# Optimization experiments

Measured on AMD Instinct MI355X. Metric: run time of the kernel, lower is better.

Reference implementation:

```python
import jax, jax.numpy as jnp
import numpy as np

HEADS = 16
D_MODEL = 1024
GROUP = 4
SEQ = 2048
HEAD_DIM = D_MODEL // HEADS          # 64
KV_HEADS = HEADS // GROUP            # 4


def rope_tables(head_dim, seq_len, base=10000.0):
    # NOTE: faithful to source: exp = -2*arange(0,d,2)/d  (steps of 2 -> base^{-4j/d})
    exp = -2.0 * jnp.arange(0, head_dim, 2, dtype=jnp.float32) / head_dim
    thetas = jnp.power(base, exp)                       # [d/2]
    m = jnp.arange(seq_len, dtype=jnp.float32)          # [S]
    freq = jnp.outer(m, thetas)                         # [S, d/2]
    return jnp.cos(freq), jnp.sin(freq)


def apply_rope(x, cos, sin):
    # x: [B,S,H,D]; complex rotation on consecutive pairs
    B, S, H, D = x.shape
    xr = x.reshape(B, S, H, D // 2, 2)
    x0, x1 = xr[..., 0], xr[..., 1]
    c = cos[None, :S, None, :]
    s = sin[None, :S, None, :]
    out = jnp.stack([x0 * c - x1 * s, x0 * s + x1 * c], axis=-1)
    return out.reshape(B, S, H, D)


def setup_inputs() -> dict:
    key = jax.random.key(0)
    ks = jax.random.split(key, 8)
    B = 1
    q = jax.random.normal(ks[0], (B, SEQ, D_MODEL), dtype=jnp.float32)
    k = jax.random.normal(ks[1], (B, SEQ, D_MODEL), dtype=jnp.float32)
    v = jax.random.normal(ks[2], (B, SEQ, D_MODEL), dtype=jnp.float32)
    mask = jnp.tril(jnp.ones((SEQ, SEQ), dtype=jnp.int32))[None]  # causal [B,S,S]
    sc = 0.02
    Wq = jax.random.normal(ks[3], (D_MODEL, D_MODEL), dtype=jnp.float32) * sc
    Wk = jax.random.normal(ks[4], (D_MODEL, D_MODEL // GROUP), dtype=jnp.float32) * sc
    Wv = jax.random.normal(ks[5], (D_MODEL, D_MODEL // GROUP), dtype=jnp.float32) * sc
    Wo = jax.random.normal(ks[6], (D_MODEL, D_MODEL), dtype=jnp.float32) * sc
    bq = jnp.zeros((D_MODEL,), jnp.float32)
    bk = jnp.zeros((D_MODEL // GROUP,), jnp.float32)
    bv = jnp.zeros((D_MODEL // GROUP,), jnp.float32)
    bo = jnp.zeros((D_MODEL,), jnp.float32)
    return {"q": q, "k": k, "v": v, "mask": mask, "Wq": Wq, "bq": bq,
            "Wk": Wk, "bk": bk, "Wv": Wv, "bv": bv, "Wo": Wo, "bo": bo}


def reference(q, k, v, mask, Wq, bq, Wk, bk, Wv, bv, Wo, bo):
    B, S, _ = q.shape
    cos, sin = rope_tables(HEAD_DIM, S)
    qh = (q @ Wq + bq).reshape(B, S, HEADS, HEAD_DIM)
    kh = (k @ Wk + bk).reshape(B, S, KV_HEADS, HEAD_DIM)
    vh = (v @ Wv + bv).reshape(B, S, KV_HEADS, HEAD_DIM)
    qh = apply_rope(qh, cos, sin)
    kh = apply_rope(kh, cos, sin)
    qh = qh.transpose(0, 2, 1, 3)                       # [B,H,S,D]
    kh = kh.transpose(0, 2, 1, 3)                       # [B,Hkv,S,D]
    vh = vh.transpose(0, 2, 1, 3)
    # torch .repeat tiles: query head j attends kv head j % KV_HEADS
    kh = jnp.tile(kh, (1, GROUP, 1, 1))                 # [B,H,S,D]
    vh = jnp.tile(vh, (1, GROUP, 1, 1))
    scores = jnp.einsum('bhqd,bhkd->bhqk', qh, kh) / jnp.sqrt(
        jnp.asarray(HEAD_DIM, dtype=qh.dtype))
    scores = jnp.where(mask[:, None, :, :] == 0, -jnp.inf, scores)
    attn = jax.nn.softmax(scores, axis=-1)
    out = jnp.einsum('bhqk,bhkd->bhqd', attn, vh)
    out = out.transpose(0, 2, 1, 3).reshape(B, S, D_MODEL)
    return out @ Wo + bo
```

## Files before the change

### kernel.cpp

```cpp
#include <hip/hip_runtime.h>
#include <hip/hip_bf16.h>
#include <math.h>


#define SEQ 2048
#define DM 1024
#define HD 64

using u16 = unsigned short;
typedef __attribute__((ext_vector_type(8))) short bf16x8;
typedef __attribute__((ext_vector_type(4))) float f32x4;

#define QSCALE 0.18033688011112042f

__device__ __forceinline__ u16 f2b(float f) {
    union { float f; unsigned int i; } v; v.f = f;
    unsigned int u = v.i;
    return (u16)((u + 0x7fffu + ((u >> 16) & 1u)) >> 16);
}
__device__ __forceinline__ u16 f2b_fast(float f) {
    union { float f; unsigned int i; } v; v.f = f;
    return (u16)((v.i + 0x8000u) >> 16);
}

__global__ __launch_bounds__(256) void prep_kernel(
    const float* __restrict__ qin, const float* __restrict__ kin, const float* __restrict__ vin,
    const float* __restrict__ Wq, const float* __restrict__ Wk,
    const float* __restrict__ Wv, const float* __restrict__ Wo,
    u16* __restrict__ Xq, u16* __restrict__ Xk, u16* __restrict__ Xv,
    u16* __restrict__ Wt, u16* __restrict__ wot)
{
    const int b = blockIdx.x;
    const int t = threadIdx.x;

    if (b < 640) {
        __shared__ short T[64][72];
        const float* W; u16* dst; int N, t0, rowoff;
        if (b < 256)      { W = Wq; dst = Wt;  N = 1024; t0 = b;       rowoff = 0; }
        else if (b < 320) { W = Wk; dst = Wt;  N = 256;  t0 = b - 256; rowoff = 1024; }
        else if (b < 384) { W = Wv; dst = Wt;  N = 256;  t0 = b - 320; rowoff = 1280; }
        else              { W = Wo; dst = wot; N = 1024; t0 = b - 384; rowoff = 0; }
        const int ntn = N >> 6;
        const int k0 = (t0 / ntn) * 64, n0 = (t0 % ntn) * 64;
        const int r = t >> 4, c4 = (t & 15) * 4;
        #pragma unroll
        for (int rr = 0; rr < 4; ++rr) {
            const int k = r + rr * 16;
            float4 w4 = *reinterpret_cast<const float4*>(W + (size_t)(k0 + k) * N + n0 + c4);
            T[c4 + 0][k] = (short)f2b(w4.x);
            T[c4 + 1][k] = (short)f2b(w4.y);
            T[c4 + 2][k] = (short)f2b(w4.z);
            T[c4 + 3][k] = (short)f2b(w4.w);
        }
        __syncthreads();
        const int n = t >> 2, ck = (t & 3) * 16;
        u16* dp = dst + (size_t)(rowoff + n0 + n) * DM + k0 + ck;
        *reinterpret_cast<bf16x8*>(dp)     = *reinterpret_cast<const bf16x8*>(&T[n][ck]);
        *reinterpret_cast<bf16x8*>(dp + 8) = *reinterpret_cast<const bf16x8*>(&T[n][ck + 8]);
    } else {
        const int idx = b - 640;
        const int which = idx >> 8;
        const int ib = idx & 255;
        const float* src = (which == 0) ? qin : (which == 1) ? kin : vin;
        u16* dst = (which == 0) ? Xq : (which == 1) ? Xk : Xv;
        const size_t base = (size_t)ib * 8192 + (size_t)t * 32;
        #pragma unroll
        for (int c = 0; c < 4; ++c) {
            float4 x0 = *reinterpret_cast<const float4*>(src + base + c * 8);
            float4 x1 = *reinterpret_cast<const float4*>(src + base + c * 8 + 4);
            bf16x8 o;
            o[0] = (short)f2b(x0.x); o[1] = (short)f2b(x0.y);
            o[2] = (short)f2b(x0.z); o[3] = (short)f2b(x0.w);
            o[4] = (short)f2b(x1.x); o[5] = (short)f2b(x1.y);
            o[6] = (short)f2b(x1.z); o[7] = (short)f2b(x1.w);
            *reinterpret_cast<bf16x8*>(dst + base + c * 8) = o;
        }
    }
}

__global__ __launch_bounds__(256) void proj_mfma(
    const u16* __restrict__ Xq, const u16* __restrict__ Xk, const u16* __restrict__ Xv,
    const u16* __restrict__ Wt,
    const float* __restrict__ bq, const float* __restrict__ bk, const float* __restrict__ bv,
    u16* __restrict__ Qr, u16* __restrict__ Kr, u16* __restrict__ Vrt)
{
    const int n0 = blockIdx.x * 64, m0 = blockIdx.y * 64;
    const int zone = (n0 < 1024) ? 0 : (n0 < 1280) ? 1 : 2;
    const u16* __restrict__ Az = (zone == 0) ? Xq : (zone == 1) ? Xk : Xv;

    __shared__ short As[64][72];
    __shared__ short Bs[64][72];

    const int t = threadIdx.x;
    const int w = t >> 6, lane = t & 63, lm = lane & 15, quad = lane >> 4;
    const int sr = t >> 2, sc = (t & 3) * 16;

    f32x4 acc[4] = { {0,0,0,0}, {0,0,0,0}, {0,0,0,0}, {0,0,0,0} };

    for (int k0 = 0; k0 < DM; k0 += 64) {
        const u16* ap = Az + (size_t)(m0 + sr) * DM + k0 + sc;
        *reinterpret_cast<bf16x8*>(&As[sr][sc])     = *reinterpret_cast<const bf16x8*>(ap);
        *reinterpret_cast<bf16x8*>(&As[sr][sc + 8]) = *reinterpret_cast<const bf16x8*>(ap + 8);
        const u16* bp = Wt + (size_t)(n0 + sr) * DM + k0 + sc;
        *reinterpret_cast<bf16x8*>(&Bs[sr][sc])     = *reinterpret_cast<const bf16x8*>(bp);
        *reinterpret_cast<bf16x8*>(&Bs[sr][sc + 8]) = *reinterpret_cast<const bf16x8*>(bp + 8);
        __syncthreads();
        bf16x8 af0 = *reinterpret_cast<const bf16x8*>(&As[16 * w + lm][quad * 8]);
        bf16x8 af1 = *reinterpret_cast<const bf16x8*>(&As[16 * w + lm][32 + quad * 8]);
        #pragma unroll
        for (int nb = 0; nb < 4; ++nb) {
            bf16x8 b0 = *reinterpret_cast<const bf16x8*>(&Bs[16 * nb + lm][quad * 8]);
            bf16x8 b1 = *reinterpret_cast<const bf16x8*>(&Bs[16 * nb + lm][32 + quad * 8]);
            acc[nb] = __builtin_amdgcn_mfma_f32_16x16x32_bf16(af0, b0, acc[nb], 0, 0, 0);
            acc[nb] = __builtin_amdgcn_mfma_f32_16x16x32_bf16(af1, b1, acc[nb], 0, 0, 0);
        }
        __syncthreads();
    }

    const float* __restrict__ bias = (zone == 0) ? bq : (zone == 1) ? bk : bv;
    const int nbase = (zone == 0) ? n0 : (zone == 1) ? (n0 - 1024) : (n0 - 1280);
    const int head = nbase >> 6;
    #pragma unroll
    for (int nb = 0; nb < 4; ++nb) {
        const int d = 16 * nb + lm;
        const float bvv = bias[nbase + d];
        float vals[4];
        #pragma unroll
        for (int r = 0; r < 4; ++r) vals[r] = acc[nb][r] + bvv;
        if (zone != 2) {
            const int pi = d >> 1;
            const float theta = exp2f(-0.8304820237f * (float)pi);
            const bool odd = (lm & 1);
            const float sca = (zone == 0) ? QSCALE : 1.0f;
            #pragma unroll
            for (int r = 0; r < 4; ++r) {
                const int m = m0 + 16 * w + quad * 4 + r;
                float sn, cs;
                sincosf((float)m * theta, &sn, &cs);
                float x  = vals[r];
                float xp = __shfl_xor(x, 1);
                vals[r] = (odd ? (xp * sn + x * cs) : (x * cs - xp * sn)) * sca;
            }
            u16* op = (zone == 0 ? Qr : Kr) + (size_t)head * SEQ * HD;
            #pragma unroll
            for (int r = 0; r < 4; ++r) {
                const int m = m0 + 16 * w + quad * 4 + r;
                op[(size_t)m * HD + d] = f2b(vals[r]);
            }
        } else {
            u16 pk[4];
            #pragma unroll
            for (int r = 0; r < 4; ++r) pk[r] = f2b(vals[r]);
            u16* vp = Vrt + ((size_t)head * HD + d) * SEQ + m0 + 16 * w + quad * 4;
            *reinterpret_cast<uint2*>(vp) = *reinterpret_cast<uint2*>(pk);
        }
    }
}

__global__ __launch_bounds__(256) void attn_mfma(
    const u16* __restrict__ Qr, const u16* __restrict__ Kr, const u16* __restrict__ Vrt,
    u16* __restrict__ AO)
{
    const int h  = blockIdx.x;
    const int qy = blockIdx.y;
    const int qt = (qy < 16) ? (2 * qy) : (63 - 2 * qy);
    const int kvh = h & 3;

    __shared__ short Qs[64][72];
    __shared__ short Ks[2][64][72];
    __shared__ short Vt[64][136];
    __shared__ short Ps[64][136];
    __shared__ float Lred[4][64];

    const int t = threadIdx.x;
    const int w = t >> 6, lane = t & 63, lm = lane & 15, quad = lane >> 4;
    const int sr = t >> 2, sc = (t & 3) * 16;
    const int colb = (sc >> 4) * 32;

    {
        const u16* qp = Qr + ((size_t)h * SEQ + qt * 64 + sr) * HD + sc;
        *reinterpret_cast<bf16x8*>(&Qs[sr][sc])     = *reinterpret_cast<const bf16x8*>(qp);
        *reinterpret_cast<bf16x8*>(&Qs[sr][sc + 8]) = *reinterpret_cast<const bf16x8*>(qp + 8);
    }
    __syncthreads();
    bf16x8 bq[4][2];
    #pragma unroll
    for (int nb = 0; nb < 4; ++nb) {
        bq[nb][0] = *reinterpret_cast<const bf16x8*>(&Qs[16 * nb + lm][quad * 8]);
        bq[nb][1] = *reinterpret_cast<const bf16x8*>(&Qs[16 * nb + lm][32 + quad * 8]);
    }

    f32x4 O[4][4];
    #pragma unroll
    for (int i = 0; i < 4; ++i)
        #pragma unroll
        for (int j = 0; j < 4; ++j) O[i][j] = (f32x4){0.f, 0.f, 0.f, 0.f};
    float lp[4] = { 0.f, 0.f, 0.f, 0.f };

    const int ntile = qt + 1;
    const u16* kbase = Kr  + ((size_t)kvh * SEQ + sr) * HD + sc;
    const u16* vbase = Vrt + ((size_t)kvh * HD  + sr) * SEQ + sc;

    for (int u = 0; u < ntile; u += 2) {
        const bool has1 = (u + 1 < ntile);
        {
            const u16* kp0 = kbase + (size_t)u * 64 * HD;
            *reinterpret_cast<bf16x8*>(&Ks[0][sr][sc])     = *reinterpret_cast<const bf16x8*>(kp0);
            *reinterpret_cast<bf16x8*>(&Ks[0][sr][sc + 8]) = *reinterpret_cast<const bf16x8*>(kp0 + 8);
            const u16* vp0 = vbase + (size_t)u * 64;
            *reinterpret_cast<bf16x8*>(&Vt[sr][colb])      = *reinterpret_cast<const bf16x8*>(vp0);
            *reinterpret_cast<bf16x8*>(&Vt[sr][colb + 8])  = *reinterpret_cast<const bf16x8*>(vp0 + 8);
            if (has1) {
                const u16* kp1 = kbase + (size_t)(u + 1) * 64 * HD;
                *reinterpret_cast<bf16x8*>(&Ks[1][sr][sc])     = *reinterpret_cast<const bf16x8*>(kp1);
                *reinterpret_cast<bf16x8*>(&Ks[1][sr][sc + 8]) = *reinterpret_cast<const bf16x8*>(kp1 + 8);
                const u16* vp1 = vbase + (size_t)(u + 1) * 64;
                *reinterpret_cast<bf16x8*>(&Vt[sr][colb + 16]) = *reinterpret_cast<const bf16x8*>(vp1);
                *reinterpret_cast<bf16x8*>(&Vt[sr][colb + 24]) = *reinterpret_cast<const bf16x8*>(vp1 + 8);
            } else {
                bf16x8 z = {0,0,0,0,0,0,0,0};
                *reinterpret_cast<bf16x8*>(&Vt[sr][colb + 16]) = z;
                *reinterpret_cast<bf16x8*>(&Vt[sr][colb + 24]) = z;
            }
        }
        __syncthreads();

        #pragma unroll
        for (int tp = 0; tp < 2; ++tp) {
            const int kt = u + tp;
            if (tp == 1 && !has1) {
                const uint2 z2 = make_uint2(0u, 0u);
                #pragma unroll
                for (int nb = 0; nb < 4; ++nb)
                    *reinterpret_cast<uint2*>(&Ps[16 * nb + lm][w * 32 + 16 + quad * 4]) = z2;
                continue;
            }
            const bf16x8 ak0 = *reinterpret_cast<const bf16x8*>(&Ks[tp][16 * w + lm][quad * 8]);
            const bf16x8 ak1 = *reinterpret_cast<const bf16x8*>(&Ks[tp][16 * w + lm][32 + quad * 8]);
            const bool diag = (kt == qt);
            #pragma unroll
            for (int nb = 0; nb < 4; ++nb) {
                f32x4 ss = { 0.f, 0.f, 0.f, 0.f };
                ss = __builtin_amdgcn_mfma_f32_16x16x32_bf16(ak0, bq[nb][0], ss, 0, 0, 0);
                ss = __builtin_amdgcn_mfma_f32_16x16x32_bf16(ak1, bq[nb][1], ss, 0, 0, 0);
                u16 pk[4];
                #pragma unroll
                for (int r = 0; r < 4; ++r) {
                    float sv = ss[r];
                    if (diag && (16 * w + quad * 4 + r > 16 * nb + lm)) sv = -INFINITY;
                    float e = __builtin_amdgcn_exp2f(fminf(sv, 126.f));
                    lp[nb] += e;
                    pk[r] = f2b_fast(e);
                }
                *reinterpret_cast<uint2*>(&Ps[16 * nb + lm][w * 32 + tp * 16 + quad * 4]) =
                    *reinterpret_cast<uint2*>(pk);
            }
        }

        #pragma unroll
        for (int db = 0; db < 4; ++db) {
            const bf16x8 av = *reinterpret_cast<const bf16x8*>(&Vt[16 * db + lm][w * 32 + quad * 8]);
            #pragma unroll
            for (int nb = 0; nb < 4; ++nb) {
                const bf16x8 bp = *reinterpret_cast<const bf16x8*>(&Ps[16 * nb + lm][w * 32 + quad * 8]);
                O[db][nb] = __builtin_amdgcn_mfma_f32_16x16x32_bf16(av, bp, O[db][nb], 0, 0, 0);
            }
        }
        __syncthreads();
    }

    #pragma unroll
    for (int nb = 0; nb < 4; ++nb) {
        lp[nb] += __shfl_xor(lp[nb], 16);
        lp[nb] += __shfl_xor(lp[nb], 32);
    }
    if (quad == 0) {
        #pragma unroll
        for (int nb = 0; nb < 4; ++nb) Lred[w][16 * nb + lm] = lp[nb];
    }

    float* Sf = reinterpret_cast<float*>(&Ps[0][0]);
    #pragma unroll
    for (int ph = 0; ph < 4; ++ph) {
        __syncthreads();
        if (w == ph) {
            #pragma unroll
            for (int db = 0; db < 4; ++db)
                #pragma unroll
                for (int nb = 0; nb < 4; ++nb)
                    #pragma unroll
                    for (int r = 0; r < 4; ++r) {
                        const int d = 16 * db + quad * 4 + r, q = 16 * nb + lm;
                        const float v = O[db][nb][r];
                        Sf[q * 68 + d] = (ph == 0) ? v : (Sf[q * 68 + d] + v);
                    }
        }
    }
    __syncthreads();

    {
        const int q = t >> 2, dc = (t & 3) * 16;
        const float linv = 1.0f / (Lred[0][q] + Lred[1][q] + Lred[2][q] + Lred[3][q]);
        u16 pk[16];
        #pragma unroll
        for (int j = 0; j < 16; ++j)
            pk[j] = f2b(Sf[q * 68 + dc + j] * linv);
        u16* op = AO + (size_t)(qt * 64 + q) * DM + h * HD + dc;
        *reinterpret_cast<bf16x8*>(op)     = *reinterpret_cast<const bf16x8*>(pk);
        *reinterpret_cast<bf16x8*>(op + 8) = *reinterpret_cast<const bf16x8*>(pk + 8);
    }
}

__global__ __launch_bounds__(256) void oproj_mfma(
    const u16* __restrict__ AO, const u16* __restrict__ wot,
    const float* __restrict__ bo, float* __restrict__ out)
{
    __shared__ short As[64][72];
    __shared__ short Bs[64][72];
    const int t = threadIdx.x;
    const int w = t >> 6, lane = t & 63, lm = lane & 15, quad = lane >> 4;
    const int m0 = blockIdx.y * 64, n0 = blockIdx.x * 64;
    const int sr = t >> 2, sc = (t & 3) * 16;

    f32x4 acc[4] = { {0,0,0,0}, {0,0,0,0}, {0,0,0,0}, {0,0,0,0} };

    for (int k0 = 0; k0 < DM; k0 += 64) {
        const u16* ap = AO + (size_t)(m0 + sr) * DM + k0 + sc;
        *reinterpret_cast<bf16x8*>(&As[sr][sc])     = *reinterpret_cast<const bf16x8*>(ap);
        *reinterpret_cast<bf16x8*>(&As[sr][sc + 8]) = *reinterpret_cast<const bf16x8*>(ap + 8);
        const u16* bp = wot + (size_t)(n0 + sr) * DM + k0 + sc;
        *reinterpret_cast<bf16x8*>(&Bs[sr][sc])     = *reinterpret_cast<const bf16x8*>(bp);
        *reinterpret_cast<bf16x8*>(&Bs[sr][sc + 8]) = *reinterpret_cast<const bf16x8*>(bp + 8);
        __syncthreads();
        bf16x8 af0 = *reinterpret_cast<const bf16x8*>(&As[16 * w + lm][quad * 8]);
        bf16x8 af1 = *reinterpret_cast<const bf16x8*>(&As[16 * w + lm][32 + quad * 8]);
        #pragma unroll
        for (int nb = 0; nb < 4; ++nb) {
            bf16x8 b0 = *reinterpret_cast<const bf16x8*>(&Bs[16 * nb + lm][quad * 8]);
            bf16x8 b1 = *reinterpret_cast<const bf16x8*>(&Bs[16 * nb + lm][32 + quad * 8]);
            acc[nb] = __builtin_amdgcn_mfma_f32_16x16x32_bf16(af0, b0, acc[nb], 0, 0, 0);
            acc[nb] = __builtin_amdgcn_mfma_f32_16x16x32_bf16(af1, b1, acc[nb], 0, 0, 0);
        }
        __syncthreads();
    }

    #pragma unroll
    for (int nb = 0; nb < 4; ++nb) {
        const int dl = 16 * nb + lm;
        const float bv = bo[n0 + dl];
        #pragma unroll
        for (int r = 0; r < 4; ++r) {
            const int m = m0 + 16 * w + quad * 4 + r;
            out[(size_t)m * DM + n0 + dl] = acc[nb][r] + bv;
        }
    }
}

extern "C" void kernel_launch(void* const* d_in, const int* in_sizes, int n_in,
                              void* d_out, int out_size, void* d_ws, size_t ws_size,
                              hipStream_t stream)
{
    const float* q  = (const float*)d_in[0];
    const float* k  = (const float*)d_in[1];
    const float* v  = (const float*)d_in[2];
    const float* Wq = (const float*)d_in[4];
    const float* bq = (const float*)d_in[5];
    const float* Wk = (const float*)d_in[6];
    const float* bk = (const float*)d_in[7];
    const float* Wv = (const float*)d_in[8];
    const float* bv = (const float*)d_in[9];
    const float* Wo = (const float*)d_in[10];
    const float* bo = (const float*)d_in[11];
    float* out = (float*)d_out;

    u16* Xq  = (u16*)d_ws;
    u16* Xk  = Xq  + (size_t)SEQ * DM;
    u16* Xv  = Xk  + (size_t)SEQ * DM;
    u16* Wt  = Xv  + (size_t)SEQ * DM;
    u16* wot = Wt  + (size_t)1536 * 1024;
    u16* Qr  = wot + (size_t)1024 * 1024;
    u16* Kr  = Qr  + (size_t)16 * SEQ * HD;
    u16* Vrt = Kr  + (size_t)4 * SEQ * HD;
    u16* AO  = Vrt + (size_t)4 * SEQ * HD;

    hipLaunchKernelGGL(prep_kernel, dim3(1408), dim3(256), 0, stream,
                       q, k, v, Wq, Wk, Wv, Wo, Xq, Xk, Xv, Wt, wot);
    hipLaunchKernelGGL(proj_mfma, dim3(24, 32), dim3(256), 0, stream,
                       Xq, Xk, Xv, Wt, bq, bk, bv, Qr, Kr, Vrt);
    hipLaunchKernelGGL(attn_mfma, dim3(16, 32), dim3(256), 0, stream,
                       Qr, Kr, Vrt, AO);
    hipLaunchKernelGGL(oproj_mfma, dim3(16, 32), dim3(256), 0, stream,
                       AO, wot, bo, out);
}
```

Before: 184.0 us.

## Restructure attention into paired-tile 512-thread blocks and prefetch GEMM tiles

Both GEMM kernels now prefetch the next K tile into registers while computing from a double-buffered LDS tile, which hides global load latency. The attention kernel is rewritten so each 512-thread block processes two complementary query tiles (qy and 31-qy) with one team of four waves each, for balanced causal work. Each wave owns 16 query rows and keeps its own P buffer, so the cross-wave O reduction through shared memory goes away. V is now stored in an interleaved permuted order to match the new PV MFMA operand layout. The risks are higher register and LDS pressure and correctness depending on that permuted V layout.

```diff
diff --git a/kernel.cpp b/kernel.cpp
--- a/kernel.cpp
+++ b/kernel.cpp
@@ -88,8 +88,8 @@
     const int zone = (n0 < 1024) ? 0 : (n0 < 1280) ? 1 : 2;
     const u16* __restrict__ Az = (zone == 0) ? Xq : (zone == 1) ? Xk : Xv;
 
-    __shared__ short As[64][72];
-    __shared__ short Bs[64][72];
+    __shared__ short As[2][64][72];
+    __shared__ short Bs[2][64][72];
 
     const int t = threadIdx.x;
     const int w = t >> 6, lane = t & 63, lm = lane & 15, quad = lane >> 4;
@@ -97,20 +97,32 @@
 
     f32x4 acc[4] = { {0,0,0,0}, {0,0,0,0}, {0,0,0,0}, {0,0,0,0} };
 
+    const u16* ap_ = Az + (size_t)(m0 + sr) * DM + sc;
+    const u16* bp_ = Wt + (size_t)(n0 + sr) * DM + sc;
+    bf16x8 aR0 = *reinterpret_cast<const bf16x8*>(ap_);
+    bf16x8 aR1 = *reinterpret_cast<const bf16x8*>(ap_ + 8);
+    bf16x8 bR0 = *reinterpret_cast<const bf16x8*>(bp_);
+    bf16x8 bR1 = *reinterpret_cast<const bf16x8*>(bp_ + 8);
+
     for (int k0 = 0; k0 < DM; k0 += 64) {
-        const u16* ap = Az + (size_t)(m0 + sr) * DM + k0 + sc;
-        *reinterpret_cast<bf16x8*>(&As[sr][sc])     = *reinterpret_cast<const bf16x8*>(ap);
-        *reinterpret_cast<bf16x8*>(&As[sr][sc + 8]) = *reinterpret_cast<const bf16x8*>(ap + 8);
-        const u16* bp = Wt + (size_t)(n0 + sr) * DM + k0 + sc;
-        *reinterpret_cast<bf16x8*>(&Bs[sr][sc])     = *reinterpret_cast<const bf16x8*>(bp);
-        *reinterpret_cast<bf16x8*>(&Bs[sr][sc + 8]) = *reinterpret_cast<const bf16x8*>(bp + 8);
-        __syncthreads();
-        bf16x8 af0 = *reinterpret_cast<const bf16x8*>(&As[16 * w + lm][quad * 8]);
-        bf16x8 af1 = *reinterpret_cast<const bf16x8*>(&As[16 * w + lm][32 + quad * 8]);
+        const int buf = (k0 >> 6) & 1;
+        *reinterpret_cast<bf16x8*>(&As[buf][sr][sc])     = aR0;
+        *reinterpret_cast<bf16x8*>(&As[buf][sr][sc + 8]) = aR1;
+        *reinterpret_cast<bf16x8*>(&Bs[buf][sr][sc])     = bR0;
+        *reinterpret_cast<bf16x8*>(&Bs[buf][sr][sc + 8]) = bR1;
+        if (k0 + 64 < DM) {
+            aR0 = *reinterpret_cast<const bf16x8*>(ap_ + k0 + 64);
+            aR1 = *reinterpret_cast<const bf16x8*>(ap_ + k0 + 72);
+            bR0 = *reinterpret_cast<const bf16x8*>(bp_ + k0 + 64);
+            bR1 = *reinterpret_cast<const bf16x8*>(bp_ + k0 + 72);
+        }
+        __syncthreads();
+        bf16x8 af0 = *reinterpret_cast<const bf16x8*>(&As[buf][16 * w + lm][quad * 8]);
+        bf16x8 af1 = *reinterpret_cast<const bf16x8*>(&As[buf][16 * w + lm][32 + quad * 8]);
         #pragma unroll
         for (int nb = 0; nb < 4; ++nb) {
-            bf16x8 b0 = *reinterpret_cast<const bf16x8*>(&Bs[16 * nb + lm][quad * 8]);
-            bf16x8 b1 = *reinterpret_cast<const bf16x8*>(&Bs[16 * nb + lm][32 + quad * 8]);
+            bf16x8 b0 = *reinterpret_cast<const bf16x8*>(&Bs[buf][16 * nb + lm][quad * 8]);
+            bf16x8 b1 = *reinterpret_cast<const bf16x8*>(&Bs[buf][16 * nb + lm][32 + quad * 8]);
             acc[nb] = __builtin_amdgcn_mfma_f32_16x16x32_bf16(af0, b0, acc[nb], 0, 0, 0);
             acc[nb] = __builtin_amdgcn_mfma_f32_16x16x32_bf16(af1, b1, acc[nb], 0, 0, 0);
         }
@@ -132,6 +144,7 @@
             const float theta = exp2f(-0.8304820237f * (float)pi);
             const bool odd = (lm & 1);
             const float sca = (zone == 0) ? QSCALE : 1.0f;
+            u16* op = (zone == 0 ? Qr : Kr) + (size_t)head * SEQ * HD;
             #pragma unroll
             for (int r = 0; r < 4; ++r) {
                 const int m = m0 + 16 * w + quad * 4 + r;
@@ -139,175 +152,122 @@
                 sincosf((float)m * theta, &sn, &cs);
                 float x  = vals[r];
                 float xp = __shfl_xor(x, 1);
-                vals[r] = (odd ? (xp * sn + x * cs) : (x * cs - xp * sn)) * sca;
-            }
-            u16* op = (zone == 0 ? Qr : Kr) + (size_t)head * SEQ * HD;
+                float o  = (odd ? (xp * sn + x * cs) : (x * cs - xp * sn)) * sca;
+                op[(size_t)m * HD + d] = f2b(o);
+            }
+        } else {
+            u16* vp = Vrt + ((size_t)head * HD + d) * SEQ;
             #pragma unroll
             for (int r = 0; r < 4; ++r) {
                 const int m = m0 + 16 * w + quad * 4 + r;
-                op[(size_t)m * HD + d] = f2b(vals[r]);
-            }
-        } else {
-            u16 pk[4];
-            #pragma unroll
-            for (int r = 0; r < 4; ++r) pk[r] = f2b(vals[r]);
-            u16* vp = Vrt + ((size_t)head * HD + d) * SEQ + m0 + 16 * w + quad * 4;
-            *reinterpret_cast<uint2*>(vp) = *reinterpret_cast<uint2*>(pk);
-        }
-    }
-}
-
-__global__ __launch_bounds__(256) void attn_mfma(
+                const int within = m & 63;
+                const int pos = (m & ~63) + 4 * (within & 15) + (within >> 4);
+                vp[pos] = f2b(vals[r]);
+            }
+        }
+    }
+}
+
+__global__ __launch_bounds__(512) void attn_mfma(
     const u16* __restrict__ Qr, const u16* __restrict__ Kr, const u16* __restrict__ Vrt,
     u16* __restrict__ AO)
 {
     const int h  = blockIdx.x;
     const int qy = blockIdx.y;
-    const int qt = (qy < 16) ? (2 * qy) : (63 - 2 * qy);
     const int kvh = h & 3;
 
-    __shared__ short Qs[64][72];
-    __shared__ short Ks[2][64][72];
-    __shared__ short Vt[64][136];
-    __shared__ short Ps[64][136];
-    __shared__ float Lred[4][64];
+    __shared__ u16 Ks[2][64][72];
+    __shared__ u16 Vt[2][64][72];
+    __shared__ u16 Ps[8][16][76];
 
     const int t = threadIdx.x;
     const int w = t >> 6, lane = t & 63, lm = lane & 15, quad = lane >> 4;
-    const int sr = t >> 2, sc = (t & 3) * 16;
-    const int colb = (sc >> 4) * 32;
+    const int team = w >> 2, wt = w & 3;
+    const int qt  = team ? (31 - qy) : qy;
+    const int qtb = 31 - qy;
 
     {
-        const u16* qp = Qr + ((size_t)h * SEQ + qt * 64 + sr) * HD + sc;
-        *reinterpret_cast<bf16x8*>(&Qs[sr][sc])     = *reinterpret_cast<const bf16x8*>(qp);
-        *reinterpret_cast<bf16x8*>(&Qs[sr][sc + 8]) = *reinterpret_cast<const bf16x8*>(qp + 8);
-    }
-    __syncthreads();
-    bf16x8 bq[4][2];
-    #pragma unroll
-    for (int nb = 0; nb < 4; ++nb) {
-        bq[nb][0] = *reinterpret_cast<const bf16x8*>(&Qs[16 * nb + lm][quad * 8]);
-        bq[nb][1] = *reinterpret_cast<const bf16x8*>(&Qs[16 * nb + lm][32 + quad * 8]);
-    }
-
-    f32x4 O[4][4];
-    #pragma unroll
-    for (int i = 0; i < 4; ++i)
-        #pragma unroll
-        for (int j = 0; j < 4; ++j) O[i][j] = (f32x4){0.f, 0.f, 0.f, 0.f};
+        const int row = lane >> 2, c = (lane & 3) * 16;
+        const u16* qp = Qr + ((size_t)h * SEQ + qt * 64 + wt * 16 + row) * HD + c;
+        *reinterpret_cast<bf16x8*>(&Ps[w][row][c])     = *reinterpret_cast<const bf16x8*>(qp);
+        *reinterpret_cast<bf16x8*>(&Ps[w][row][c + 8]) = *reinterpret_cast<const bf16x8*>(qp + 8);
+    }
+    const bf16x8 aq0 = *reinterpret_cast<const bf16x8*>(&Ps[w][lm][quad * 8]);
+    const bf16x8 aq1 = *reinterpret_cast<const bf16x8*>(&Ps[w][lm][32 + quad * 8]);
+
+    f32x4 O[4] = { {0,0,0,0}, {0,0,0,0}, {0,0,0,0}, {0,0,0,0} };
     float lp[4] = { 0.f, 0.f, 0.f, 0.f };
 
-    const int ntile = qt + 1;
-    const u16* kbase = Kr  + ((size_t)kvh * SEQ + sr) * HD + sc;
-    const u16* vbase = Vrt + ((size_t)kvh * HD  + sr) * SEQ + sc;
-
-    for (int u = 0; u < ntile; u += 2) {
-        const bool has1 = (u + 1 < ntile);
-        {
-            const u16* kp0 = kbase + (size_t)u * 64 * HD;
-            *reinterpret_cast<bf16x8*>(&Ks[0][sr][sc])     = *reinterpret_cast<const bf16x8*>(kp0);
-            *reinterpret_cast<bf16x8*>(&Ks[0][sr][sc + 8]) = *reinterpret_cast<const bf16x8*>(kp0 + 8);
-            const u16* vp0 = vbase + (size_t)u * 64;
-            *reinterpret_cast<bf16x8*>(&Vt[sr][colb])      = *reinterpret_cast<const bf16x8*>(vp0);
-            *reinterpret_cast<bf16x8*>(&Vt[sr][colb + 8])  = *reinterpret_cast<const bf16x8*>(vp0 + 8);
-            if (has1) {
-                const u16* kp1 = kbase + (size_t)(u + 1) * 64 * HD;
-                *reinterpret_cast<bf16x8*>(&Ks[1][sr][sc])     = *reinterpret_cast<const bf16x8*>(kp1);
-                *reinterpret_cast<bf16x8*>(&Ks[1][sr][sc + 8]) = *reinterpret_cast<const bf16x8*>(kp1 + 8);
-                const u16* vp1 = vbase + (size_t)(u + 1) * 64;
-                *reinterpret_cast<bf16x8*>(&Vt[sr][colb + 16]) = *reinterpret_cast<const bf16x8*>(vp1);
-                *reinterpret_cast<bf16x8*>(&Vt[sr][colb + 24]) = *reinterpret_cast<const bf16x8*>(vp1 + 8);
-            } else {
-                bf16x8 z = {0,0,0,0,0,0,0,0};
-                *reinterpret_cast<bf16x8*>(&Vt[sr][colb + 16]) = z;
-                *reinterpret_cast<bf16x8*>(&Vt[sr][colb + 24]) = z;
-            }
-        }
-        __syncthreads();
-
-        #pragma unroll
-        for (int tp = 0; tp < 2; ++tp) {
-            const int kt = u + tp;
-            if (tp == 1 && !has1) {
-                const uint2 z2 = make_uint2(0u, 0u);
-                #pragma unroll
-                for (int nb = 0; nb < 4; ++nb)
-                    *reinterpret_cast<uint2*>(&Ps[16 * nb + lm][w * 32 + 16 + quad * 4]) = z2;
-                continue;
-            }
-            const bf16x8 ak0 = *reinterpret_cast<const bf16x8*>(&Ks[tp][16 * w + lm][quad * 8]);
-            const bf16x8 ak1 = *reinterpret_cast<const bf16x8*>(&Ks[tp][16 * w + lm][32 + quad * 8]);
-            const bool diag = (kt == qt);
+    const int srow = t >> 3, sc2 = (t & 7) * 8;
+    const u16* kb_ = Kr  + ((size_t)kvh * SEQ + srow) * HD + sc2;
+    const u16* vb_ = Vrt + ((size_t)kvh * HD + srow) * SEQ + sc2;
+    bf16x8 kR = *reinterpret_cast<const bf16x8*>(kb_);
+    bf16x8 vR = *reinterpret_cast<const bf16x8*>(vb_);
+
+    for (int kt = 0; kt <= qtb; ++kt) {
+        const int buf = kt & 1;
+        *reinterpret_cast<bf16x8*>(&Ks[buf][srow][sc2]) = kR;
+        *reinterpret_cast<bf16x8*>(&Vt[buf][srow][sc2]) = vR;
+        if (kt < qtb) {
+            kR = *reinterpret_cast<const bf16x8*>(kb_ + (size_t)(kt + 1) * 64 * HD);
+            vR = *reinterpret_cast<const bf16x8*>(vb_ + (size_t)(kt + 1) * 64);
+        }
+        __syncthreads();
+
+        if (kt <= qt) {
+            f32x4 s[4];
             #pragma unroll
             for (int nb = 0; nb < 4; ++nb) {
-                f32x4 ss = { 0.f, 0.f, 0.f, 0.f };
-                ss = __builtin_amdgcn_mfma_f32_16x16x32_bf16(ak0, bq[nb][0], ss, 0, 0, 0);
-                ss = __builtin_amdgcn_mfma_f32_16x16x32_bf16(ak1, bq[nb][1], ss, 0, 0, 0);
-                u16 pk[4];
-                #pragma unroll
-                for (int r = 0; r < 4; ++r) {
-                    float sv = ss[r];
-                    if (diag && (16 * w + quad * 4 + r > 16 * nb + lm)) sv = -INFINITY;
-                    float e = __builtin_amdgcn_exp2f(fminf(sv, 126.f));
-                    lp[nb] += e;
-                    pk[r] = f2b_fast(e);
-                }
-                *reinterpret_cast<uint2*>(&Ps[16 * nb + lm][w * 32 + tp * 16 + quad * 4]) =
-                    *reinterpret_cast<uint2*>(pk);
-            }
-        }
-
-        #pragma unroll
-        for (int db = 0; db < 4; ++db) {
-            const bf16x8 av = *reinterpret_cast<const bf16x8*>(&Vt[16 * db + lm][w * 32 + quad * 8]);
-            #pragma unroll
-            for (int nb = 0; nb < 4; ++nb) {
-                const bf16x8 bp = *reinterpret_cast<const bf16x8*>(&Ps[16 * nb + lm][w * 32 + quad * 8]);
-                O[db][nb] = __builtin_amdgcn_mfma_f32_16x16x32_bf16(av, bp, O[db][nb], 0, 0, 0);
-            }
-        }
-        __syncthreads();
-    }
-
-    #pragma unroll
-    for (int nb = 0; nb < 4; ++nb) {
-        lp[nb] += __shfl_xor(lp[nb], 16);
-        lp[nb] += __shfl_xor(lp[nb], 32);
-    }
-    if (quad == 0) {
-        #pragma unroll
-        for (int nb = 0; nb < 4; ++nb) Lred[w][16 * nb + lm] = lp[nb];
-    }
-
-    float* Sf = reinterpret_cast<float*>(&Ps[0][0]);
-    #pragma unroll
-    for (int ph = 0; ph < 4; ++ph) {
-        __syncthreads();
-        if (w == ph) {
-            #pragma unroll
-            for (int db = 0; db < 4; ++db)
+                bf16x8 b0 = *reinterpret_cast<const bf16x8*>(&Ks[buf][16 * nb + lm][quad * 8]);
+                bf16x8 b1 = *reinterpret_cast<const bf16x8*>(&Ks[buf][16 * nb + lm][32 + quad * 8]);
+                f32x4 zz = { 0.f, 0.f, 0.f, 0.f };
+                zz = __builtin_amdgcn_mfma_f32_16x16x32_bf16(aq0, b0, zz, 0, 0, 0);
+                s[nb] = __builtin_amdgcn_mfma_f32_16x16x32_bf16(aq1, b1, zz, 0, 0, 0);
+            }
+
+            if (kt == qt) {
                 #pragma unroll
                 for (int nb = 0; nb < 4; ++nb)
                     #pragma unroll
-                    for (int r = 0; r < 4; ++r) {
-                        const int d = 16 * db + quad * 4 + r, q = 16 * nb + lm;
-                        const float v = O[db][nb][r];
-                        Sf[q * 68 + d] = (ph == 0) ? v : (Sf[q * 68 + d] + v);
-                    }
-        }
-    }
-    __syncthreads();
-
-    {
-        const int q = t >> 2, dc = (t & 3) * 16;
-        const float linv = 1.0f / (Lred[0][q] + Lred[1][q] + Lred[2][q] + Lred[3][q]);
-        u16 pk[16];
-        #pragma unroll
-        for (int j = 0; j < 16; ++j)
-            pk[j] = f2b(Sf[q * 68 + dc + j] * linv);
-        u16* op = AO + (size_t)(qt * 64 + q) * DM + h * HD + dc;
-        *reinterpret_cast<bf16x8*>(op)     = *reinterpret_cast<const bf16x8*>(pk);
-        *reinterpret_cast<bf16x8*>(op + 8) = *reinterpret_cast<const bf16x8*>(pk + 8);
+                    for (int r = 0; r < 4; ++r)
+                        if (16 * nb + lm > 16 * wt + quad * 4 + r) s[nb][r] = -INFINITY;
+            }
+
+            #pragma unroll
+            for (int r = 0; r < 4; ++r) {
+                u16 pk[4];
+                #pragma unroll
+                for (int nb = 0; nb < 4; ++nb) {
+                    float e = __builtin_amdgcn_exp2f(fminf(s[nb][r], 126.f));
+                    lp[r] += e;
+                    pk[nb] = f2b_fast(e);
+                }
+                *reinterpret_cast<uint2*>(&Ps[w][quad * 4 + r][4 * lm]) =
+                    *reinterpret_cast<uint2*>(pk);
+            }
+
+            const bf16x8 ap0 = *reinterpret_cast<const bf16x8*>(&Ps[w][lm][quad * 8]);
+            const bf16x8 ap1 = *reinterpret_cast<const bf16x8*>(&Ps[w][lm][32 + quad * 8]);
+            #pragma unroll
+            for (int db = 0; db < 4; ++db) {
+                bf16x8 v0 = *reinterpret_cast<const bf16x8*>(&Vt[buf][16 * db + lm][quad * 8]);
+                bf16x8 v1 = *reinterpret_cast<const bf16x8*>(&Vt[buf][16 * db + lm][32 + quad * 8]);
+                O[db] = __builtin_amdgcn_mfma_f32_16x16x32_bf16(ap0, v0, O[db], 0, 0, 0);
+                O[db] = __builtin_amdgcn_mfma_f32_16x16x32_bf16(ap1, v1, O[db], 0, 0, 0);
+            }
+        }
+    }
+
+    #pragma unroll
+    for (int r = 0; r < 4; ++r) {
+        #pragma unroll
+        for (int off = 1; off < 16; off <<= 1)
+            lp[r] += __shfl_xor(lp[r], off);
+        const float inv = 1.0f / lp[r];
+        const size_t row = (size_t)(qt * 64 + 16 * wt + quad * 4 + r) * DM + (size_t)h * HD;
+        #pragma unroll
+        for (int db = 0; db < 4; ++db)
+            AO[row + 16 * db + lm] = f2b(O[db][r] * inv);
     }
 }
 
@@ -315,8 +275,8 @@
     const u16* __restrict__ AO, const u16* __restrict__ wot,
     const float* __restrict__ bo, float* __restrict__ out)
 {
-    __shared__ short As[64][72];
-    __shared__ short Bs[64][72];
+    __shared__ short As[2][64][72];
+    __shared__ short Bs[2][64][72];
     const int t = threadIdx.x;
     const int w = t >> 6, lane = t & 63, lm = lane & 15, quad = lane >> 4;
     const int m0 = blockIdx.y * 64, n0 = blockIdx.x * 64;
@@ -324,20 +284,32 @@
 
     f32x4 acc[4] = { {0,0,0,0}, {0,0,0,0}, {0,0,0,0}, {0,0,0,0} };
 
+    const u16* ap_ = AO  + (size_t)(m0 + sr) * DM + sc;
+    const u16* bp_ = wot + (size_t)(n0 + sr) * DM + sc;
+    bf16x8 aR0 = *reinterpret_cast<const bf16x8*>(ap_);
+    bf16x8 aR1 = *reinterpret_cast<const bf16x8*>(ap_ + 8);
+    bf16x8 bR0 = *reinterpret_cast<const bf16x8*>(bp_);
+    bf16x8 bR1 = *reinterpret_cast<const bf16x8*>(bp_ + 8);
+
     for (int k0 = 0; k0 < DM; k0 += 64) {
-        const u16* ap = AO + (size_t)(m0 + sr) * DM + k0 + sc;
-        *reinterpret_cast<bf16x8*>(&As[sr][sc])     = *reinterpret_cast<const bf16x8*>(ap);
-        *reinterpret_cast<bf16x8*>(&As[sr][sc + 8]) = *reinterpret_cast<const bf16x8*>(ap + 8);
-        const u16* bp = wot + (size_t)(n0 + sr) * DM + k0 + sc;
-        *reinterpret_cast<bf16x8*>(&Bs[sr][sc])     = *reinterpret_cast<const bf16x8*>(bp);
-        *reinterpret_cast<bf16x8*>(&Bs[sr][sc + 8]) = *reinterpret_cast<const bf16x8*>(bp + 8);
-        __syncthreads();
-        bf16x8 af0 = *reinterpret_cast<const bf16x8*>(&As[16 * w + lm][quad * 8]);
-        bf16x8 af1 = *reinterpret_cast<const bf16x8*>(&As[16 * w + lm][32 + quad * 8]);
+        const int buf = (k0 >> 6) & 1;
+        *reinterpret_cast<bf16x8*>(&As[buf][sr][sc])     = aR0;
+        *reinterpret_cast<bf16x8*>(&As[buf][sr][sc + 8]) = aR1;
+        *reinterpret_cast<bf16x8*>(&Bs[buf][sr][sc])     = bR0;
+        *reinterpret_cast<bf16x8*>(&Bs[buf][sr][sc + 8]) = bR1;
+        if (k0 + 64 < DM) {
+            aR0 = *reinterpret_cast<const bf16x8*>(ap_ + k0 + 64);
+            aR1 = *reinterpret_cast<const bf16x8*>(ap_ + k0 + 72);
+            bR0 = *reinterpret_cast<const bf16x8*>(bp_ + k0 + 64);
+            bR1 = *reinterpret_cast<const bf16x8*>(bp_ + k0 + 72);
+        }
+        __syncthreads();
+        bf16x8 af0 = *reinterpret_cast<const bf16x8*>(&As[buf][16 * w + lm][quad * 8]);
+        bf16x8 af1 = *reinterpret_cast<const bf16x8*>(&As[buf][16 * w + lm][32 + quad * 8]);
         #pragma unroll
         for (int nb = 0; nb < 4; ++nb) {
-            bf16x8 b0 = *reinterpret_cast<const bf16x8*>(&Bs[16 * nb + lm][quad * 8]);
-            bf16x8 b1 = *reinterpret_cast<const bf16x8*>(&Bs[16 * nb + lm][32 + quad * 8]);
+            bf16x8 b0 = *reinterpret_cast<const bf16x8*>(&Bs[buf][16 * nb + lm][quad * 8]);
+            bf16x8 b1 = *reinterpret_cast<const bf16x8*>(&Bs[buf][16 * nb + lm][32 + quad * 8]);
             acc[nb] = __builtin_amdgcn_mfma_f32_16x16x32_bf16(af0, b0, acc[nb], 0, 0, 0);
             acc[nb] = __builtin_amdgcn_mfma_f32_16x16x32_bf16(af1, b1, acc[nb], 0, 0, 0);
         }
@@ -387,7 +359,7 @@
                        q, k, v, Wq, Wk, Wv, Wo, Xq, Xk, Xv, Wt, wot);
     hipLaunchKernelGGL(proj_mfma, dim3(24, 32), dim3(256), 0, stream,
                        Xq, Xk, Xv, Wt, bq, bk, bv, Qr, Kr, Vrt);
-    hipLaunchKernelGGL(attn_mfma, dim3(16, 32), dim3(256), 0, stream,
+    hipLaunchKernelGGL(attn_mfma, dim3(16, 16), dim3(512), 0, stream,
                        Qr, Kr, Vrt, AO);
     hipLaunchKernelGGL(oproj_mfma, dim3(16, 32), dim3(256), 0, stream,
                        AO, wot, bo, out);
```

New measurement: 166.3 us. 9.6% less time.
